# Optimization experiments

Measured on AMD Instinct MI355X. Metric: run time of the kernel, lower is better.

The kernel has to match this reference:

```python
import jax, jax.numpy as jnp
import numpy as np

# dims
BB, T, D_IN = 16, 2048, 64
D = 512          # hidden_dim (d_model)
DI = 2 * D       # d_inner (expand=2)
N = 16           # d_state
DC = 4           # d_conv
R = D // 16      # dt_rank = 32
L = 3            # n_layer
D_OUT = 128


def setup_inputs() -> dict:
    key = jax.random.key(0)
    ks = jax.random.split(key, 10)
    g = lambda k, shape, s: (jax.random.normal(k, shape, jnp.float32) * s)
    A_log = jnp.tile(jnp.log(jnp.arange(1, N + 1, dtype=jnp.float32))[None, None, :], (L, DI, 1))
    return {
        "x": g(ks[0], (BB, T, D_IN), 1.0),
        "Wi": g(ks[1], (D, D_IN), 0.05), "bi": jnp.zeros((D,), jnp.float32),
        "Win": g(ks[2], (L, 2 * DI, D), 0.02),
        "convw": g(ks[3], (L, DI, DC), 0.2), "convb": jnp.zeros((L, DI), jnp.float32),
        "Wx": g(ks[4], (L, R + 2 * N, DI), 0.02),
        "Wdt": g(ks[5], (L, DI, R), 0.05), "bdt": jnp.full((L, DI), -1.0, jnp.float32),
        "A_log": A_log, "Dp": jnp.ones((L, DI), jnp.float32),
        "Wout": g(ks[6], (L, D, DI), 0.02),
        "Wo": g(ks[7], (D_OUT, D), 0.05), "bo": jnp.zeros((D_OUT,), jnp.float32),
    }


def _selective_scan(u, delta, A, Bm, Cm, Dv):
    # u, delta: [B,T,DI]; A: [DI,N]; Bm, Cm: [B,T,N]; Dv: [DI]
    def step(h, inp):
        d_t, u_t, B_t, C_t = inp  # [B,DI],[B,DI],[B,N],[B,N]
        dA = jnp.exp(d_t[:, :, None] * A)                      # [B,DI,N]
        h = dA * h + (d_t * u_t)[:, :, None] * B_t[:, None, :]  # [B,DI,N]
        y = jnp.einsum('bdn,bn->bd', h, C_t)
        return h, y

    h0 = jnp.zeros((u.shape[0], u.shape[2], A.shape[1]), u.dtype)
    xs = (delta.transpose(1, 0, 2), u.transpose(1, 0, 2),
          Bm.transpose(1, 0, 2), Cm.transpose(1, 0, 2))
    _, ys = jax.lax.scan(step, h0, xs)
    return ys.transpose(1, 0, 2) + u * Dv


def _mamba_layer(x, Win, cw, cb, Wx, Wdt, bdt, A_log, Dv, Wout):
    xz = x @ Win.T                      # [B,T,2*DI]
    xin, z = jnp.split(xz, 2, axis=-1)
    # causal depthwise conv1d
    xc = jax.lax.conv_general_dilated(
        xin.transpose(0, 2, 1), cw[:, None, :], (1,), [(DC - 1, 0)],
        feature_group_count=DI, dimension_numbers=('NCH', 'OIH', 'NCH'))
    u = jax.nn.silu((xc + cb[None, :, None]).transpose(0, 2, 1))  # [B,T,DI]
    dbc = u @ Wx.T                      # [B,T,R+2N]
    dt, Bm, Cm = dbc[..., :R], dbc[..., R:R + N], dbc[..., R + N:]
    delta = jax.nn.softplus(dt @ Wdt.T + bdt)
    A = -jnp.exp(A_log)
    y = _selective_scan(u, delta, A, Bm, Cm, Dv)
    return (y * jax.nn.silu(z)) @ Wout.T


def reference(x, Wi, bi, Win, convw, convb, Wx, Wdt, bdt, A_log, Dp, Wout, Wo, bo):
    h = x @ Wi.T + bi
    for l in range(L):
        h = _mamba_layer(h, Win[l], convw[l], convb[l], Wx[l], Wdt[l], bdt[l],
                         A_log[l], Dp[l], Wout[l])
    return jnp.tanh(h @ Wo.T + bo)  # [B,T,output_dim]
```

## Files before the change

### kernel.cpp

```cpp
#include <hip/hip_runtime.h>
#include <hip/hip_bf16.h>

#define BB_ 16
#define T_ 2048
#define DIN_ 64
#define D_ 512
#define DI_ 1024
#define N_ 16
#define DC_ 4
#define R_ 32
#define L_ 3
#define DOUT_ 128
#define CL_ 64
#define NCH_ (T_ / CL_)

typedef __attribute__((ext_vector_type(8))) _Float16 f16x8;
typedef __attribute__((ext_vector_type(4))) float f32x4;

__device__ __forceinline__ float silu_f(float x) { return x / (1.f + __expf(-x)); }

__device__ __forceinline__ float softplus_f(float t) {
    return fmaxf(t, 0.f) + __logf(1.f + __expf(-fabsf(t)));
}

__device__ __forceinline__ unsigned short f2h(float f) {
    union { _Float16 h; unsigned short u; } c;
    c.h = (_Float16)f;
    return c.u;
}

__device__ __forceinline__ void gload_lds16(const unsigned short* g,
                                            unsigned short* l) {
    __builtin_amdgcn_global_load_lds(
        (const __attribute__((address_space(1))) void*)g,
        (__attribute__((address_space(3))) void*)l, 16, 0, 0);
}

__device__ __forceinline__ float decode_scale(unsigned int bits) {
    if (bits == 0u) return 1.f;
    const int E = (int)(bits >> 23) & 0xFF;
    return __uint_as_float((unsigned)(265 - E) << 23);
}

__device__ __forceinline__ uint4 pack8(float4 lo, float4 hi, float s) {
    union { uint4 u; unsigned short h[8]; } r;
    r.h[0] = f2h(lo.x * s); r.h[1] = f2h(lo.y * s);
    r.h[2] = f2h(lo.z * s); r.h[3] = f2h(lo.w * s);
    r.h[4] = f2h(hi.x * s); r.h[5] = f2h(hi.y * s);
    r.h[6] = f2h(hi.z * s); r.h[7] = f2h(hi.w * s);
    return r.u;
}

__device__ __forceinline__ const float* wregion(
    int r, const float* Win, const float* Wout, const float* Wx,
    const float* Wo, size_t* n4)
{
    if (r < 3)       { *n4 = 262144; return Win  + (size_t)r * 1048576; }
    else if (r < 6)  { *n4 = 131072; return Wout + (size_t)(r - 3) * 524288; }
    else if (r == 6) { *n4 = 16384;  return Wo; }
    else             { *n4 = 16384;  return Wx  + (size_t)(r - 7) * 65536; }
}

__global__ __launch_bounds__(256) void amax_all(
    const float* __restrict__ Win, const float* __restrict__ Wout,
    const float* __restrict__ Wx, const float* __restrict__ Wo,
    unsigned int* __restrict__ scales)
{
    size_t n4;
    const float* p = wregion(blockIdx.z, Win, Wout, Wx, Wo, &n4);
    float m = 0.f;
    for (size_t i = (size_t)blockIdx.x * 256 + threadIdx.x; i < n4;
         i += (size_t)gridDim.x * 256) {
        const float4 v = ((const float4*)p)[i];
        m = fmaxf(m, fmaxf(fmaxf(fabsf(v.x), fabsf(v.y)),
                           fmaxf(fabsf(v.z), fabsf(v.w))));
    }
#pragma unroll
    for (int off = 32; off; off >>= 1) m = fmaxf(m, __shfl_down(m, off));
    __shared__ float sm[4];
    if ((threadIdx.x & 63) == 0) sm[threadIdx.x >> 6] = m;
    __syncthreads();
    if (threadIdx.x == 0) {
        const float b = fmaxf(fmaxf(sm[0], sm[1]), fmaxf(sm[2], sm[3]));
        atomicMax(scales + blockIdx.z, __float_as_uint(b));
    }
}

__global__ __launch_bounds__(256) void cast_all(
    const float* __restrict__ Win, const float* __restrict__ Wout,
    const float* __restrict__ Wx, const float* __restrict__ Wo,
    unsigned short* __restrict__ WinH, unsigned short* __restrict__ WoutH,
    unsigned short* __restrict__ WxH, unsigned short* __restrict__ WoH,
    const unsigned int* __restrict__ scales)
{
    const int r = blockIdx.z;
    size_t n4;
    const float* p = wregion(r, Win, Wout, Wx, Wo, &n4);
    unsigned short* o;
    if (r < 3)       o = WinH  + (size_t)r * 1048576;
    else if (r < 6)  o = WoutH + (size_t)(r - 3) * 524288;
    else if (r == 6) o = WoH;
    else             o = WxH   + (size_t)(r - 7) * 65536;
    const float s = decode_scale(scales[r]);
    for (size_t i = (size_t)blockIdx.x * 256 + threadIdx.x; i < n4;
         i += (size_t)gridDim.x * 256) {
        const float4 v = ((const float4*)p)[i];
        ((ushort4*)o)[i] = make_ushort4(f2h(v.x * s), f2h(v.y * s),
                                        f2h(v.z * s), f2h(v.w * s));
    }
}

template<int ACT>
__global__ __launch_bounds__(256) void gemm_f32a_t128(
    const float* __restrict__ A, int lda,
    const unsigned short* __restrict__ B, int ldb,
    const float* __restrict__ bias,
    float* __restrict__ C, int ldc, int K,
    const unsigned int* __restrict__ sa, const unsigned int* __restrict__ sb,
    unsigned int* __restrict__ oamax)
{
    __shared__ __align__(16) unsigned short As[128 * 32];
    __shared__ __align__(16) unsigned short Bs[2][128 * 32];
    const int tid  = threadIdx.x;
    const int lane = tid & 63;
    const int w    = tid >> 6;
    const int wr   = (w >> 1) << 6;
    const int wc   = (w & 1) << 6;
    const int l15  = lane & 15, l4 = lane >> 4;
    const int row0 = blockIdx.y << 7, col0 = blockIdx.x << 7;
    const int tq   = tid >> 2;
    const int tr   = (tid & 3) << 3;

    const float sA  = decode_scale(*sa);
    const float inv = (1.f / sA) * (1.f / decode_scale(*sb));

    const float* Ar0 = A + (size_t)(row0 + tq) * lda + tr;
    const float* Ar1 = A + (size_t)(row0 + 64 + tq) * lda + tr;
    const unsigned short* Br0 = B + (size_t)(col0 + tq) * ldb + tr;
    const unsigned short* Br1 = B + (size_t)(col0 + 64 + tq) * ldb + tr;

    f32x4 acc[4][4];
#pragma unroll
    for (int m = 0; m < 4; ++m)
#pragma unroll
        for (int n = 0; n < 4; ++n) acc[m][n] = (f32x4){0.f, 0.f, 0.f, 0.f};

    float4 a0lo = *(const float4*)(Ar0), a0hi = *(const float4*)(Ar0 + 4);
    float4 a1lo = *(const float4*)(Ar1), a1hi = *(const float4*)(Ar1 + 4);
    gload_lds16(Br0, &Bs[0][tq * 32 + tr]);
    gload_lds16(Br1, &Bs[0][(64 + tq) * 32 + tr]);

    int cur = 0;
    for (int k0 = 0; k0 < K; k0 += 32) {
        __syncthreads();
        *(uint4*)&As[tq * 32 + tr]        = pack8(a0lo, a0hi, sA);
        *(uint4*)&As[(64 + tq) * 32 + tr] = pack8(a1lo, a1hi, sA);
        __syncthreads();

        if (k0 + 32 < K) {
            gload_lds16(Br0 + k0 + 32, &Bs[cur ^ 1][tq * 32 + tr]);
            gload_lds16(Br1 + k0 + 32, &Bs[cur ^ 1][(64 + tq) * 32 + tr]);
            a0lo = *(const float4*)(Ar0 + k0 + 32);
            a0hi = *(const float4*)(Ar0 + k0 + 36);
            a1lo = *(const float4*)(Ar1 + k0 + 32);
            a1hi = *(const float4*)(Ar1 + k0 + 36);
        }

        f16x8 af[4], bfr[4];
#pragma unroll
        for (int m = 0; m < 4; ++m)
            af[m] = *(const f16x8*)&As[(wr + m * 16 + l15) * 32 + l4 * 8];
#pragma unroll
        for (int n = 0; n < 4; ++n)
            bfr[n] = *(const f16x8*)&Bs[cur][(wc + n * 16 + l15) * 32 + l4 * 8];
#pragma unroll
        for (int m = 0; m < 4; ++m)
#pragma unroll
            for (int n = 0; n < 4; ++n)
                acc[m][n] = __builtin_amdgcn_mfma_f32_16x16x32_f16(
                    af[m], bfr[n], acc[m][n], 0, 0, 0);
        cur ^= 1;
    }

    float am = 0.f;
#pragma unroll
    for (int n = 0; n < 4; ++n) {
        const int col = col0 + wc + n * 16 + l15;
        float bc = 0.f;
        if (ACT == 3) bc = bias[col];
#pragma unroll
        for (int m = 0; m < 4; ++m) {
            const int rowb = row0 + wr + m * 16 + (l4 << 2);
#pragma unroll
            for (int r = 0; r < 4; ++r) {
                float v = acc[m][n][r] * inv;
                if (ACT == 3) v = tanhf(v + bc);
                C[(size_t)(rowb + r) * ldc + col] = v;
                am = fmaxf(am, fabsf(v));
            }
        }
    }
    if (oamax) {
#pragma unroll
        for (int off = 32; off; off >>= 1) am = fmaxf(am, __shfl_down(am, off));
        if (lane == 0) atomicMax(oamax, __float_as_uint(am));
    }
}

__global__ __launch_bounds__(256) void gemm_f16u_t64n(
    const float* __restrict__ A, int lda,
    const unsigned short* __restrict__ B, int ldb,
    float* __restrict__ C, int ldc, int K,
    const unsigned int* __restrict__ sa, const unsigned int* __restrict__ sb)
{
    __shared__ __align__(16) unsigned short As[128 * 32];
    __shared__ __align__(16) unsigned short Bs[64 * 32];
    const int tid  = threadIdx.x;
    const int lane = tid & 63;
    const int w    = tid >> 6;
    const int l15  = lane & 15, l4 = lane >> 4;
    const int row0 = blockIdx.y << 7;
    const int tq   = tid >> 2;
    const int tr   = (tid & 3) << 3;

    const float sA  = decode_scale(*sa);
    const float inv = (1.f / sA) * (1.f / decode_scale(*sb));

    const float* Ar0 = A + (size_t)(row0 + tq) * lda + tr;
    const float* Ar1 = A + (size_t)(row0 + 64 + tq) * lda + tr;
    const unsigned short* Br = B + (size_t)tq * ldb + tr;

    f32x4 acc[2][4];
#pragma unroll
    for (int m = 0; m < 2; ++m)
#pragma unroll
        for (int n = 0; n < 4; ++n) acc[m][n] = (f32x4){0.f, 0.f, 0.f, 0.f};

    float4 a0lo = *(const float4*)(Ar0), a0hi = *(const float4*)(Ar0 + 4);
    float4 a1lo = *(const float4*)(Ar1), a1hi = *(const float4*)(Ar1 + 4);
    uint4  bv   = *(const uint4*)(Br);

    for (int k0 = 0; k0 < K; k0 += 32) {
        __syncthreads();
        *(uint4*)&As[tq * 32 + tr]        = pack8(a0lo, a0hi, sA);
        *(uint4*)&As[(64 + tq) * 32 + tr] = pack8(a1lo, a1hi, sA);
        *(uint4*)&Bs[tq * 32 + tr]        = bv;
        __syncthreads();

        if (k0 + 32 < K) {
            a0lo = *(const float4*)(Ar0 + k0 + 32);
            a0hi = *(const float4*)(Ar0 + k0 + 36);
            a1lo = *(const float4*)(Ar1 + k0 + 32);
            a1hi = *(const float4*)(Ar1 + k0 + 36);
            bv   = *(const uint4*)(Br  + k0 + 32);
        }

        f16x8 af[2], bfr[4];
#pragma unroll
        for (int m = 0; m < 2; ++m)
            af[m] = *(const f16x8*)&As[(w * 32 + m * 16 + l15) * 32 + l4 * 8];
#pragma unroll
        for (int n = 0; n < 4; ++n)
            bfr[n] = *(const f16x8*)&Bs[(n * 16 + l15) * 32 + l4 * 8];
#pragma unroll
        for (int m = 0; m < 2; ++m)
#pragma unroll
            for (int n = 0; n < 4; ++n)
                acc[m][n] = __builtin_amdgcn_mfma_f32_16x16x32_f16(
                    af[m], bfr[n], acc[m][n], 0, 0, 0);
    }

#pragma unroll
    for (int n = 0; n < 4; ++n) {
        const int col = n * 16 + l15;
#pragma unroll
        for (int m = 0; m < 2; ++m) {
            const int rowb = row0 + w * 32 + m * 16 + (l4 << 2);
#pragma unroll
            for (int r = 0; r < 4; ++r)
                C[(size_t)(rowb + r) * ldc + col] = acc[m][n][r] * inv;
        }
    }
}

__global__ __launch_bounds__(256) void gemm_in(
    const float* __restrict__ A, int lda,
    const float* __restrict__ B, int ldb,
    const float* __restrict__ bias,
    float* __restrict__ C, int ldc, int K,
    unsigned int* __restrict__ oamax)
{
    __shared__ __align__(16) float As[8][128];
    __shared__ __align__(16) float Bs[8][128];
    const int tid  = threadIdx.x;
    const int row0 = blockIdx.y << 7;
    const int col0 = blockIdx.x << 7;
    const int tx = tid & 15, ty = tid >> 4;

    float acc[8][8];
#pragma unroll
    for (int i = 0; i < 8; ++i)
#pragma unroll
        for (int j = 0; j < 8; ++j) acc[i][j] = 0.f;

    const int arow = tid >> 1;
    const int acol = (tid & 1) << 2;
    const float* Ap = A + (size_t)(row0 + arow) * lda + acol;
    const float* Bp = B + (size_t)(col0 + arow) * ldb + acol;

    for (int k0 = 0; k0 < K; k0 += 8) {
        const float4 av = *(const float4*)(Ap + k0);
        const float4 bv = *(const float4*)(Bp + k0);
        __syncthreads();
        As[acol + 0][arow] = av.x; As[acol + 1][arow] = av.y;
        As[acol + 2][arow] = av.z; As[acol + 3][arow] = av.w;
        Bs[acol + 0][arow] = bv.x; Bs[acol + 1][arow] = bv.y;
        Bs[acol + 2][arow] = bv.z; Bs[acol + 3][arow] = bv.w;
        __syncthreads();
#pragma unroll
        for (int k = 0; k < 8; ++k) {
            float a[8], b[8];
            *(float4*)&a[0] = *(const float4*)&As[k][ty << 3];
            *(float4*)&a[4] = *(const float4*)&As[k][(ty << 3) + 4];
            *(float4*)&b[0] = *(const float4*)&Bs[k][tx << 3];
            *(float4*)&b[4] = *(const float4*)&Bs[k][(tx << 3) + 4];
#pragma unroll
            for (int i = 0; i < 8; ++i)
#pragma unroll
                for (int j = 0; j < 8; ++j)
                    acc[i][j] = fmaf(a[i], b[j], acc[i][j]);
        }
    }

    float bv8[8];
#pragma unroll
    for (int j = 0; j < 8; ++j) bv8[j] = bias[col0 + (tx << 3) + j];

    float am = 0.f;
#pragma unroll
    for (int i = 0; i < 8; ++i) {
        float v[8];
#pragma unroll
        for (int j = 0; j < 8; ++j) {
            v[j] = acc[i][j] + bv8[j];
            am = fmaxf(am, fabsf(v[j]));
        }
        float* Cp = C + (size_t)(row0 + (ty << 3) + i) * ldc + col0 + (tx << 3);
        *(float4*)(Cp)     = make_float4(v[0], v[1], v[2], v[3]);
        *(float4*)(Cp + 4) = make_float4(v[4], v[5], v[6], v[7]);
    }
#pragma unroll
    for (int off = 32; off; off >>= 1) am = fmaxf(am, __shfl_down(am, off));
    if ((tid & 63) == 0) atomicMax(oamax, __float_as_uint(am));
}

__global__ __launch_bounds__(256) void conv_silu_kernel(
    const float* __restrict__ xz, const float* __restrict__ cw,
    const float* __restrict__ cb, float* __restrict__ u,
    size_t total4, unsigned int* __restrict__ uamax)
{
    float am = 0.f;
    for (size_t i = (size_t)blockIdx.x * 256 + threadIdx.x; i < total4;
         i += (size_t)gridDim.x * 256) {
        const size_t e = i * 4;
        const int c = (int)(e & (DI_ - 1));
        const size_t m = e >> 10;
        const int t = (int)(m & (T_ - 1));
        const float* xr = xz + m * 2048 + c;
        const float4 zero = make_float4(0.f, 0.f, 0.f, 0.f);
        const float4 x0 = (t >= 3) ? *(const float4*)(xr - 3 * 2048) : zero;
        const float4 x1 = (t >= 2) ? *(const float4*)(xr - 2 * 2048) : zero;
        const float4 x2 = (t >= 1) ? *(const float4*)(xr - 1 * 2048) : zero;
        const float4 x3 = *(const float4*)(xr);
        const float4 cbv = *(const float4*)(cb + c);
        const float4 w0 = *(const float4*)(cw + (size_t)c * 4);
        const float4 w1 = *(const float4*)(cw + (size_t)(c + 1) * 4);
        const float4 w2 = *(const float4*)(cw + (size_t)(c + 2) * 4);
        const float4 w3 = *(const float4*)(cw + (size_t)(c + 3) * 4);
        float4 r;
        r.x = silu_f(fmaf(x3.x, w0.w, fmaf(x2.x, w0.z, fmaf(x1.x, w0.y, fmaf(x0.x, w0.x, cbv.x)))));
        r.y = silu_f(fmaf(x3.y, w1.w, fmaf(x2.y, w1.z, fmaf(x1.y, w1.y, fmaf(x0.y, w1.x, cbv.y)))));
        r.z = silu_f(fmaf(x3.z, w2.w, fmaf(x2.z, w2.z, fmaf(x1.z, w2.y, fmaf(x0.z, w2.x, cbv.z)))));
        r.w = silu_f(fmaf(x3.w, w3.w, fmaf(x2.w, w3.z, fmaf(x1.w, w3.y, fmaf(x0.w, w3.x, cbv.w)))));
        *(float4*)(u + e) = r;
        am = fmaxf(am, fmaxf(fmaxf(fabsf(r.x), fabsf(r.y)),
                             fmaxf(fabsf(r.z), fabsf(r.w))));
    }
#pragma unroll
    for (int off = 32; off; off >>= 1) am = fmaxf(am, __shfl_down(am, off));
    __shared__ float sm[4];
    if ((threadIdx.x & 63) == 0) sm[threadIdx.x >> 6] = am;
    __syncthreads();
    if (threadIdx.x == 0) {
        const float b = fmaxf(fmaxf(sm[0], sm[1]), fmaxf(sm[2], sm[3]));
        atomicMax(uamax, __float_as_uint(b));
    }
}


__device__ __forceinline__ bool geo_check(const float* a2) {
    bool ok = true;
#pragma unroll
    for (int n = 1; n < N_; ++n)
        ok = ok && (fabsf(a2[n] - a2[0] * (n + 1)) <=
                    1e-5f * fmaxf(1.f, fabsf(a2[n])));
    return ok;
}

__global__ __launch_bounds__(256) void scan_pass1(
    const float* __restrict__ u, const float* __restrict__ dbc,
    const float* __restrict__ A_log_l, const float* __restrict__ Wdt_l,
    const float* __restrict__ bdt_l,
    float* __restrict__ P, float* __restrict__ S)
{
    __shared__ __align__(16) float sAll[CL_][64];
    const int tid = threadIdx.x;
    const int b = blockIdx.x, ch = blockIdx.z;
    const int d = (blockIdx.y << 8) + tid;

    float a2[N_], hs[N_];
#pragma unroll
    for (int n = 0; n < N_; ++n) {
        a2[n] = -__expf(A_log_l[d * N_ + n]) * 1.44269504f;
        hs[n] = 0.f;
    }
    const bool geo = geo_check(a2);
    float wdt[32];
#pragma unroll
    for (int k = 0; k < 32; k += 4)
        *(float4*)&wdt[k] = *(const float4*)(Wdt_l + (size_t)d * 32 + k);
    const float bdt_d = bdt_l[d];

    const size_t base64 = ((size_t)b * T_ + (size_t)ch * CL_) * 64;
    float* sflat = &sAll[0][0];
    for (int i = tid; i < CL_ * 64; i += 256) sflat[i] = dbc[base64 + i];
    __syncthreads();

    float sdl = 0.f;
    if (geo) {
        for (int tt = 0; tt < CL_; ++tt) {
            float t = bdt_d;
#pragma unroll
            for (int k = 0; k < 32; k += 4) {
                const float4 dv = *(const float4*)&sAll[tt][k];
                t = fmaf(dv.x, wdt[k + 0], t);
                t = fmaf(dv.y, wdt[k + 1], t);
                t = fmaf(dv.z, wdt[k + 2], t);
                t = fmaf(dv.w, wdt[k + 3], t);
            }
            const float dl = softplus_f(t);
            sdl += dl;
            const size_t m = (size_t)b * T_ + ch * CL_ + tt;
            const float du = dl * u[m * DI_ + d];
            const float r = exp2f(dl * a2[0]);
            float dA = r;
#pragma unroll
            for (int n = 0; n < N_; ++n) {
                hs[n] = fmaf(dA, hs[n], du * sAll[tt][32 + n]);
                dA *= r;
            }
        }
    } else {
        for (int tt = 0; tt < CL_; ++tt) {
            float t = bdt_d;
#pragma unroll
            for (int k = 0; k < 32; k += 4) {
                const float4 dv = *(const float4*)&sAll[tt][k];
                t = fmaf(dv.x, wdt[k + 0], t);
                t = fmaf(dv.y, wdt[k + 1], t);
                t = fmaf(dv.z, wdt[k + 2], t);
                t = fmaf(dv.w, wdt[k + 3], t);
            }
            const float dl = softplus_f(t);
            sdl += dl;
            const size_t m = (size_t)b * T_ + ch * CL_ + tt;
            const float du = dl * u[m * DI_ + d];
#pragma unroll
            for (int n = 0; n < N_; ++n) {
                const float dA = exp2f(dl * a2[n]);
                hs[n] = fmaf(dA, hs[n], du * sAll[tt][32 + n]);
            }
        }
    }
#pragma unroll
    for (int n = 0; n < N_; ++n) {
        const size_t idx = (size_t)(((b * NCH_ + ch) * N_ + n) << 10) + d;
        P[idx] = exp2f(sdl * a2[n]);
        S[idx] = hs[n];
    }
}

__global__ __launch_bounds__(256) void scan_carry(
    const float* __restrict__ P, float* __restrict__ S)
{
    const size_t gid = (size_t)blockIdx.x * 256 + threadIdx.x;
    const int d = (int)(gid & 1023);
    const int n = (int)((gid >> 10) & 15);
    const int b = (int)(gid >> 14);
    float hc = 0.f;
    for (int ch = 0; ch < NCH_; ++ch) {
        const size_t idx = (size_t)(((b * NCH_ + ch) * N_ + n) << 10) + d;
        const float p = P[idx], s = S[idx];
        S[idx] = hc;
        hc = fmaf(p, hc, s);
    }
}

__global__ __launch_bounds__(256) void scan_pass3(
    float* __restrict__ xz, const float* __restrict__ u,
    const float* __restrict__ dbc, const float* __restrict__ A_log_l,
    const float* __restrict__ Wdt_l, const float* __restrict__ bdt_l,
    const float* __restrict__ Dp_l, const float* __restrict__ S,
    unsigned int* __restrict__ gmax)
{
    __shared__ __align__(16) float sAll[CL_][64];
    const int tid = threadIdx.x;
    const int b = blockIdx.x, ch = blockIdx.z;
    const int d = (blockIdx.y << 8) + tid;

    float a2[N_], hs[N_];
#pragma unroll
    for (int n = 0; n < N_; ++n) {
        a2[n] = -__expf(A_log_l[d * N_ + n]) * 1.44269504f;
        hs[n] = S[(size_t)(((b * NCH_ + ch) * N_ + n) << 10) + d];
    }
    const bool geo = geo_check(a2);
    float wdt[32];
#pragma unroll
    for (int k = 0; k < 32; k += 4)
        *(float4*)&wdt[k] = *(const float4*)(Wdt_l + (size_t)d * 32 + k);
    const float bdt_d = bdt_l[d];
    const float Dpd = Dp_l[d];

    const size_t base64 = ((size_t)b * T_ + (size_t)ch * CL_) * 64;
    float* sflat = &sAll[0][0];
    for (int i = tid; i < CL_ * 64; i += 256) sflat[i] = dbc[base64 + i];
    __syncthreads();

    float gm = 0.f;
    if (geo) {
        for (int tt = 0; tt < CL_; ++tt) {
            float t = bdt_d;
#pragma unroll
            for (int k = 0; k < 32; k += 4) {
                const float4 dv = *(const float4*)&sAll[tt][k];
                t = fmaf(dv.x, wdt[k + 0], t);
                t = fmaf(dv.y, wdt[k + 1], t);
                t = fmaf(dv.z, wdt[k + 2], t);
                t = fmaf(dv.w, wdt[k + 3], t);
            }
            const float dl = softplus_f(t);
            const size_t m = (size_t)b * T_ + ch * CL_ + tt;
            const float uv = u[m * DI_ + d];
            const float du = dl * uv;
            const float r = exp2f(dl * a2[0]);
            float dA = r;
            float yv = 0.f;
#pragma unroll
            for (int n = 0; n < N_; ++n) {
                hs[n] = fmaf(dA, hs[n], du * sAll[tt][32 + n]);
                yv = fmaf(hs[n], sAll[tt][48 + n], yv);
                dA *= r;
            }
            yv = fmaf(uv, Dpd, yv);
            const float g = yv * silu_f(xz[m * 2048 + DI_ + d]);
            xz[m * 2048 + d] = g;
            gm = fmaxf(gm, fabsf(g));
        }
    } else {
        for (int tt = 0; tt < CL_; ++tt) {
            float t = bdt_d;
#pragma unroll
            for (int k = 0; k < 32; k += 4) {
                const float4 dv = *(const float4*)&sAll[tt][k];
                t = fmaf(dv.x, wdt[k + 0], t);
                t = fmaf(dv.y, wdt[k + 1], t);
                t = fmaf(dv.z, wdt[k + 2], t);
                t = fmaf(dv.w, wdt[k + 3], t);
            }
            const float dl = softplus_f(t);
            const size_t m = (size_t)b * T_ + ch * CL_ + tt;
            const float uv = u[m * DI_ + d];
            const float du = dl * uv;
            float yv = 0.f;
#pragma unroll
            for (int n = 0; n < N_; ++n) {
                const float dA = exp2f(dl * a2[n]);
                hs[n] = fmaf(dA, hs[n], du * sAll[tt][32 + n]);
                yv = fmaf(hs[n], sAll[tt][48 + n], yv);
            }
            yv = fmaf(uv, Dpd, yv);
            const float g = yv * silu_f(xz[m * 2048 + DI_ + d]);
            xz[m * 2048 + d] = g;
            gm = fmaxf(gm, fabsf(g));
        }
    }
#pragma unroll
    for (int off = 32; off; off >>= 1) gm = fmaxf(gm, __shfl_down(gm, off));
    if ((tid & 63) == 0) atomicMax(gmax, __float_as_uint(gm));
}

extern "C" void kernel_launch(void* const* d_in, const int* in_sizes, int n_in,
                              void* d_out, int out_size, void* d_ws, size_t ws_size,
                              hipStream_t stream) {
    const float* x     = (const float*)d_in[0];
    const float* Wi    = (const float*)d_in[1];
    const float* bi    = (const float*)d_in[2];
    const float* Win   = (const float*)d_in[3];
    const float* convw = (const float*)d_in[4];
    const float* convb = (const float*)d_in[5];
    const float* Wx    = (const float*)d_in[6];
    const float* Wdt   = (const float*)d_in[7];
    const float* bdt   = (const float*)d_in[8];
    const float* A_log = (const float*)d_in[9];
    const float* Dp    = (const float*)d_in[10];
    const float* Wout  = (const float*)d_in[11];
    const float* Wo    = (const float*)d_in[12];
    const float* bo    = (const float*)d_in[13];
    float* out = (float*)d_out;

    const size_t rowf = 3648;
    const size_t wextra =
        (3 * 1048576 + 3 * 524288 + 65536 + 3 * 65536) / 2 + 32;
    int CB = BB_;
    while (CB > 1 && ((size_t)CB * T_ * rowf + wextra) * sizeof(float) > ws_size) CB >>= 1;
    const size_t Mc = (size_t)CB * T_;

    const dim3 blk(256);
    const int rowTiles = (int)(Mc / 128);

    float* ws   = (float*)d_ws;
    float* xz   = ws;
    float* u    = xz + Mc * 2048;
    float* dbc  = u  + Mc * 1024;
    float* hPS  = dbc + Mc * 64;
    float* hb   = hPS;
    float* Pbuf = hPS;
    float* Sbuf = hPS + (size_t)CB * NCH_ * N_ * DI_;
    unsigned short* WinH  = (unsigned short*)(hPS + Mc * 512);
    unsigned short* WoutH = WinH + 3 * 1048576;
    unsigned short* WoH   = WoutH + 3 * 524288;
    unsigned short* WxH   = WoH + 65536;
    unsigned int* scales  = (unsigned int*)(WxH + 3 * 65536);

    hipMemsetAsync(scales, 0, 32 * sizeof(unsigned int), stream);

    amax_all<<<dim3(128, 1, 10), blk, 0, stream>>>(Win, Wout, Wx, Wo, scales);
    cast_all<<<dim3(64, 1, 10), blk, 0, stream>>>(
        Win, Wout, Wx, Wo, WinH, WoutH, WxH, WoH, scales);

    for (int c = 0; c < BB_ / CB; ++c) {
        const float* x_c = x + (size_t)c * Mc * DIN_;
        float* out_c     = out + (size_t)c * Mc * DOUT_;

        hipMemsetAsync(scales + 10, 0, 10 * sizeof(unsigned int), stream);

        gemm_in<<<dim3(D_ / 128, rowTiles), blk, 0, stream>>>(
            x_c, DIN_, Wi, DIN_, bi, hb, D_, DIN_, scales + 10);

        for (int l = 0; l < L_; ++l) {
            const float* cw_l   = convw + (size_t)l * DI_ * DC_;
            const float* cb_l   = convb + (size_t)l * DI_;
            const float* Wdt_l  = Wdt  + (size_t)l * DI_ * R_;
            const float* bdt_l  = bdt  + (size_t)l * DI_;
            const float* Alog_l = A_log + (size_t)l * DI_ * N_;
            const float* Dp_l   = Dp   + (size_t)l * DI_;

            gemm_f32a_t128<0><<<dim3(2048 / 128, rowTiles), blk, 0, stream>>>(
                hb, D_, WinH + (size_t)l * 1048576, D_, nullptr,
                xz, 2048, D_, scales + 10 + l, scales + l, nullptr);

            conv_silu_kernel<<<dim3(2048), blk, 0, stream>>>(
                xz, cw_l, cb_l, u, Mc * DI_ / 4, scales + 17 + l);

            gemm_f16u_t64n<<<dim3(1, rowTiles), blk, 0, stream>>>(
                u, DI_, WxH + (size_t)l * 65536, DI_, dbc, 64, DI_,
                scales + 17 + l, scales + 7 + l);

            scan_pass1<<<dim3(CB, DI_ / 256, NCH_), blk, 0, stream>>>(
                u, dbc, Alog_l, Wdt_l, bdt_l, Pbuf, Sbuf);
            scan_carry<<<dim3(CB * 64), blk, 0, stream>>>(Pbuf, Sbuf);
            scan_pass3<<<dim3(CB, DI_ / 256, NCH_), blk, 0, stream>>>(
                xz, u, dbc, Alog_l, Wdt_l, bdt_l, Dp_l, Sbuf, scales + 14 + l);

            gemm_f32a_t128<0><<<dim3(D_ / 128, rowTiles), blk, 0, stream>>>(
                xz, 2048, WoutH + (size_t)l * 524288, DI_, nullptr,
                hb, D_, DI_, scales + 14 + l, scales + 3 + l, scales + 11 + l);
        }

        gemm_f32a_t128<3><<<dim3(DOUT_ / 128, rowTiles), blk, 0, stream>>>(
            hb, D_, WoH, D_, bo, out_c, DOUT_, D_,
            scales + 13, scales + 6, nullptr);
    }
}
```

Measured before the change: 2.594 ms.

## Fuse causal conv+SiLU into x-projection GEMM and scan passes, drop u buffer

Removes the standalone conv_silu kernel and the materialized u tensor. The conv and SiLU are recomputed inside the Wx GEMM's A-tile load and again inside both scan passes from xz. The quantization scale for u now comes from an analytic upper bound (|cb| plus the sum of |w| times amax of xz) rather than the true amax. The gated output goes to a separate compact gbuf, so the out-projection reads a contiguous DI-stride buffer. This trades a full write and read of u for redundant conv arithmetic, extra strided xz reads, and a looser fp16 scale that may cost precision.

```diff
diff --git a/kernel.cpp b/kernel.cpp
--- a/kernel.cpp
+++ b/kernel.cpp
@@ -110,6 +110,28 @@
     }
 }
 
+__global__ __launch_bounds__(256) void ubound_kernel(
+    const float* __restrict__ cw, const float* __restrict__ cb,
+    const unsigned int* __restrict__ xzslot, unsigned int* __restrict__ uslot)
+{
+    const float amx = __uint_as_float(*xzslot);
+    float m = 0.f;
+    for (int c = threadIdx.x; c < DI_; c += 256) {
+        const float4 w = *(const float4*)(cw + (size_t)c * 4);
+        const float sw = fabsf(w.x) + fabsf(w.y) + fabsf(w.z) + fabsf(w.w);
+        m = fmaxf(m, fabsf(cb[c]) + sw * amx);
+    }
+#pragma unroll
+    for (int off = 32; off; off >>= 1) m = fmaxf(m, __shfl_down(m, off));
+    __shared__ float sm[4];
+    if ((threadIdx.x & 63) == 0) sm[threadIdx.x >> 6] = m;
+    __syncthreads();
+    if (threadIdx.x == 0) {
+        const float b = fmaxf(fmaxf(sm[0], sm[1]), fmaxf(sm[2], sm[3]));
+        atomicMax(uslot, __float_as_uint(b));
+    }
+}
+
 template<int ACT>
 __global__ __launch_bounds__(256) void gemm_f32a_t128(
     const float* __restrict__ A, int lda,
@@ -207,11 +229,45 @@
     }
 }
 
-__global__ __launch_bounds__(256) void gemm_f16u_t64n(
-    const float* __restrict__ A, int lda,
+__device__ __forceinline__ uint4 conv_row8(
+    const float* __restrict__ xz, int m, int c0,
+    const float* __restrict__ cw, const float* __restrict__ cb, float s)
+{
+    const int t = m & (T_ - 1);
+    const float* xr = xz + (size_t)m * 2048 + c0;
+    float x[4][8];
+#pragma unroll
+    for (int k = 0; k < 4; ++k) {
+        const int dt = 3 - k;
+        if (t >= dt) {
+            *(float4*)&x[k][0] = *(const float4*)(xr - (size_t)dt * 2048);
+            *(float4*)&x[k][4] = *(const float4*)(xr - (size_t)dt * 2048 + 4);
+        } else {
+#pragma unroll
+            for (int j = 0; j < 8; ++j) x[k][j] = 0.f;
+        }
+    }
+    union { uint4 u; unsigned short h[8]; } r;
+#pragma unroll
+    for (int j = 0; j < 8; ++j) {
+        const int c = c0 + j;
+        const float4 w = *(const float4*)(cw + (size_t)c * 4);
+        float cv = cb[c];
+        cv = fmaf(x[0][j], w.x, cv);
+        cv = fmaf(x[1][j], w.y, cv);
+        cv = fmaf(x[2][j], w.z, cv);
+        cv = fmaf(x[3][j], w.w, cv);
+        r.h[j] = f2h(silu_f(cv) * s);
+    }
+    return r.u;
+}
+
+__global__ __launch_bounds__(256) void gemm_conv_t64n(
+    const float* __restrict__ xz,
     const unsigned short* __restrict__ B, int ldb,
+    const float* __restrict__ cw, const float* __restrict__ cb,
     float* __restrict__ C, int ldc, int K,
-    const unsigned int* __restrict__ sa, const unsigned int* __restrict__ sb)
+    const unsigned int* __restrict__ su, const unsigned int* __restrict__ sb)
 {
     __shared__ __align__(16) unsigned short As[128 * 32];
     __shared__ __align__(16) unsigned short Bs[64 * 32];
@@ -223,11 +279,9 @@
     const int tq   = tid >> 2;
     const int tr   = (tid & 3) << 3;
 
-    const float sA  = decode_scale(*sa);
-    const float inv = (1.f / sA) * (1.f / decode_scale(*sb));
-
-    const float* Ar0 = A + (size_t)(row0 + tq) * lda + tr;
-    const float* Ar1 = A + (size_t)(row0 + 64 + tq) * lda + tr;
+    const float sU  = decode_scale(*su);
+    const float inv = (1.f / sU) * (1.f / decode_scale(*sb));
+
     const unsigned short* Br = B + (size_t)tq * ldb + tr;
 
     f32x4 acc[2][4];
@@ -236,24 +290,18 @@
 #pragma unroll
         for (int n = 0; n < 4; ++n) acc[m][n] = (f32x4){0.f, 0.f, 0.f, 0.f};
 
-    float4 a0lo = *(const float4*)(Ar0), a0hi = *(const float4*)(Ar0 + 4);
-    float4 a1lo = *(const float4*)(Ar1), a1hi = *(const float4*)(Ar1 + 4);
-    uint4  bv   = *(const uint4*)(Br);
+    uint4 bv = *(const uint4*)(Br);
 
     for (int k0 = 0; k0 < K; k0 += 32) {
+        const uint4 a0 = conv_row8(xz, row0 + tq, k0 + tr, cw, cb, sU);
+        const uint4 a1 = conv_row8(xz, row0 + 64 + tq, k0 + tr, cw, cb, sU);
         __syncthreads();
-        *(uint4*)&As[tq * 32 + tr]        = pack8(a0lo, a0hi, sA);
-        *(uint4*)&As[(64 + tq) * 32 + tr] = pack8(a1lo, a1hi, sA);
+        *(uint4*)&As[tq * 32 + tr]        = a0;
+        *(uint4*)&As[(64 + tq) * 32 + tr] = a1;
         *(uint4*)&Bs[tq * 32 + tr]        = bv;
         __syncthreads();
 
-        if (k0 + 32 < K) {
-            a0lo = *(const float4*)(Ar0 + k0 + 32);
-            a0hi = *(const float4*)(Ar0 + k0 + 36);
-            a1lo = *(const float4*)(Ar1 + k0 + 32);
-            a1hi = *(const float4*)(Ar1 + k0 + 36);
-            bv   = *(const uint4*)(Br  + k0 + 32);
-        }
+        if (k0 + 32 < K) bv = *(const uint4*)(Br + k0 + 32);
 
         f16x8 af[2], bfr[4];
 #pragma unroll
@@ -354,49 +402,6 @@
     if ((tid & 63) == 0) atomicMax(oamax, __float_as_uint(am));
 }
 
-__global__ __launch_bounds__(256) void conv_silu_kernel(
-    const float* __restrict__ xz, const float* __restrict__ cw,
-    const float* __restrict__ cb, float* __restrict__ u,
-    size_t total4, unsigned int* __restrict__ uamax)
-{
-    float am = 0.f;
-    for (size_t i = (size_t)blockIdx.x * 256 + threadIdx.x; i < total4;
-         i += (size_t)gridDim.x * 256) {
-        const size_t e = i * 4;
-        const int c = (int)(e & (DI_ - 1));
-        const size_t m = e >> 10;
-        const int t = (int)(m & (T_ - 1));
-        const float* xr = xz + m * 2048 + c;
-        const float4 zero = make_float4(0.f, 0.f, 0.f, 0.f);
-        const float4 x0 = (t >= 3) ? *(const float4*)(xr - 3 * 2048) : zero;
-        const float4 x1 = (t >= 2) ? *(const float4*)(xr - 2 * 2048) : zero;
-        const float4 x2 = (t >= 1) ? *(const float4*)(xr - 1 * 2048) : zero;
-        const float4 x3 = *(const float4*)(xr);
-        const float4 cbv = *(const float4*)(cb + c);
-        const float4 w0 = *(const float4*)(cw + (size_t)c * 4);
-        const float4 w1 = *(const float4*)(cw + (size_t)(c + 1) * 4);
-        const float4 w2 = *(const float4*)(cw + (size_t)(c + 2) * 4);
-        const float4 w3 = *(const float4*)(cw + (size_t)(c + 3) * 4);
-        float4 r;
-        r.x = silu_f(fmaf(x3.x, w0.w, fmaf(x2.x, w0.z, fmaf(x1.x, w0.y, fmaf(x0.x, w0.x, cbv.x)))));
-        r.y = silu_f(fmaf(x3.y, w1.w, fmaf(x2.y, w1.z, fmaf(x1.y, w1.y, fmaf(x0.y, w1.x, cbv.y)))));
-        r.z = silu_f(fmaf(x3.z, w2.w, fmaf(x2.z, w2.z, fmaf(x1.z, w2.y, fmaf(x0.z, w2.x, cbv.z)))));
-        r.w = silu_f(fmaf(x3.w, w3.w, fmaf(x2.w, w3.z, fmaf(x1.w, w3.y, fmaf(x0.w, w3.x, cbv.w)))));
-        *(float4*)(u + e) = r;
-        am = fmaxf(am, fmaxf(fmaxf(fabsf(r.x), fabsf(r.y)),
-                             fmaxf(fabsf(r.z), fabsf(r.w))));
-    }
-#pragma unroll
-    for (int off = 32; off; off >>= 1) am = fmaxf(am, __shfl_down(am, off));
-    __shared__ float sm[4];
-    if ((threadIdx.x & 63) == 0) sm[threadIdx.x >> 6] = am;
-    __syncthreads();
-    if (threadIdx.x == 0) {
-        const float b = fmaxf(fmaxf(sm[0], sm[1]), fmaxf(sm[2], sm[3]));
-        atomicMax(uamax, __float_as_uint(b));
-    }
-}
-
 
 __device__ __forceinline__ bool geo_check(const float* a2) {
     bool ok = true;
@@ -408,9 +413,10 @@
 }
 
 __global__ __launch_bounds__(256) void scan_pass1(
-    const float* __restrict__ u, const float* __restrict__ dbc,
+    const float* __restrict__ xz, const float* __restrict__ dbc,
     const float* __restrict__ A_log_l, const float* __restrict__ Wdt_l,
-    const float* __restrict__ bdt_l,
+    const float* __restrict__ bdt_l, const float* __restrict__ cw_l,
+    const float* __restrict__ cb_l,
     float* __restrict__ P, float* __restrict__ S)
 {
     __shared__ __align__(16) float sAll[CL_][64];
@@ -430,28 +436,40 @@
     for (int k = 0; k < 32; k += 4)
         *(float4*)&wdt[k] = *(const float4*)(Wdt_l + (size_t)d * 32 + k);
     const float bdt_d = bdt_l[d];
-
-    const size_t base64 = ((size_t)b * T_ + (size_t)ch * CL_) * 64;
+    const float4 cwv = *(const float4*)(cw_l + (size_t)d * 4);
+    const float cbd = cb_l[d];
+
+    const size_t mB = (size_t)b * T_ + (size_t)ch * CL_;
+    const int t0 = ch * CL_;
+    float xm1 = (t0 >= 1) ? xz[(mB - 1) * 2048 + d] : 0.f;
+    float xm2 = (t0 >= 2) ? xz[(mB - 2) * 2048 + d] : 0.f;
+    float xm3 = (t0 >= 3) ? xz[(mB - 3) * 2048 + d] : 0.f;
+
+    const size_t base64 = mB * 64;
     float* sflat = &sAll[0][0];
     for (int i = tid; i < CL_ * 64; i += 256) sflat[i] = dbc[base64 + i];
     __syncthreads();
 
     float sdl = 0.f;
-    if (geo) {
-        for (int tt = 0; tt < CL_; ++tt) {
-            float t = bdt_d;
-#pragma unroll
-            for (int k = 0; k < 32; k += 4) {
-                const float4 dv = *(const float4*)&sAll[tt][k];
-                t = fmaf(dv.x, wdt[k + 0], t);
-                t = fmaf(dv.y, wdt[k + 1], t);
-                t = fmaf(dv.z, wdt[k + 2], t);
-                t = fmaf(dv.w, wdt[k + 3], t);
-            }
-            const float dl = softplus_f(t);
-            sdl += dl;
-            const size_t m = (size_t)b * T_ + ch * CL_ + tt;
-            const float du = dl * u[m * DI_ + d];
+    for (int tt = 0; tt < CL_; ++tt) {
+        float t = bdt_d;
+#pragma unroll
+        for (int k = 0; k < 32; k += 4) {
+            const float4 dv = *(const float4*)&sAll[tt][k];
+            t = fmaf(dv.x, wdt[k + 0], t);
+            t = fmaf(dv.y, wdt[k + 1], t);
+            t = fmaf(dv.z, wdt[k + 2], t);
+            t = fmaf(dv.w, wdt[k + 3], t);
+        }
+        const float dl = softplus_f(t);
+        sdl += dl;
+        const size_t m = mB + tt;
+        const float xc = xz[m * 2048 + d];
+        float cv = fmaf(xc, cwv.w, fmaf(xm1, cwv.z,
+                    fmaf(xm2, cwv.y, fmaf(xm3, cwv.x, cbd))));
+        const float du = dl * silu_f(cv);
+        xm3 = xm2; xm2 = xm1; xm1 = xc;
+        if (geo) {
             const float r = exp2f(dl * a2[0]);
             float dA = r;
 #pragma unroll
@@ -459,22 +477,7 @@
                 hs[n] = fmaf(dA, hs[n], du * sAll[tt][32 + n]);
                 dA *= r;
             }
-        }
-    } else {
-        for (int tt = 0; tt < CL_; ++tt) {
-            float t = bdt_d;
-#pragma unroll
-            for (int k = 0; k < 32; k += 4) {
-                const float4 dv = *(const float4*)&sAll[tt][k];
-                t = fmaf(dv.x, wdt[k + 0], t);
-                t = fmaf(dv.y, wdt[k + 1], t);
-                t = fmaf(dv.z, wdt[k + 2], t);
-                t = fmaf(dv.w, wdt[k + 3], t);
-            }
-            const float dl = softplus_f(t);
-            sdl += dl;
-            const size_t m = (size_t)b * T_ + ch * CL_ + tt;
-            const float du = dl * u[m * DI_ + d];
+        } else {
 #pragma unroll
             for (int n = 0; n < N_; ++n) {
                 const float dA = exp2f(dl * a2[n]);
@@ -507,9 +510,10 @@
 }
 
 __global__ __launch_bounds__(256) void scan_pass3(
-    float* __restrict__ xz, const float* __restrict__ u,
+    const float* __restrict__ xz, float* __restrict__ g,
     const float* __restrict__ dbc, const float* __restrict__ A_log_l,
     const float* __restrict__ Wdt_l, const float* __restrict__ bdt_l,
+    const float* __restrict__ cw_l, const float* __restrict__ cb_l,
     const float* __restrict__ Dp_l, const float* __restrict__ S,
     unsigned int* __restrict__ gmax)
 {
@@ -530,70 +534,62 @@
     for (int k = 0; k < 32; k += 4)
         *(float4*)&wdt[k] = *(const float4*)(Wdt_l + (size_t)d * 32 + k);
     const float bdt_d = bdt_l[d];
+    const float4 cwv = *(const float4*)(cw_l + (size_t)d * 4);
+    const float cbd = cb_l[d];
     const float Dpd = Dp_l[d];
 
-    const size_t base64 = ((size_t)b * T_ + (size_t)ch * CL_) * 64;
+    const size_t mB = (size_t)b * T_ + (size_t)ch * CL_;
+    const int t0 = ch * CL_;
+    float xm1 = (t0 >= 1) ? xz[(mB - 1) * 2048 + d] : 0.f;
+    float xm2 = (t0 >= 2) ? xz[(mB - 2) * 2048 + d] : 0.f;
+    float xm3 = (t0 >= 3) ? xz[(mB - 3) * 2048 + d] : 0.f;
+
+    const size_t base64 = mB * 64;
     float* sflat = &sAll[0][0];
     for (int i = tid; i < CL_ * 64; i += 256) sflat[i] = dbc[base64 + i];
     __syncthreads();
 
     float gm = 0.f;
-    if (geo) {
-        for (int tt = 0; tt < CL_; ++tt) {
-            float t = bdt_d;
-#pragma unroll
-            for (int k = 0; k < 32; k += 4) {
-                const float4 dv = *(const float4*)&sAll[tt][k];
-                t = fmaf(dv.x, wdt[k + 0], t);
-                t = fmaf(dv.y, wdt[k + 1], t);
-                t = fmaf(dv.z, wdt[k + 2], t);
-                t = fmaf(dv.w, wdt[k + 3], t);
-            }
-            const float dl = softplus_f(t);
-            const size_t m = (size_t)b * T_ + ch * CL_ + tt;
-            const float uv = u[m * DI_ + d];
-            const float du = dl * uv;
+    for (int tt = 0; tt < CL_; ++tt) {
+        float t = bdt_d;
+#pragma unroll
+        for (int k = 0; k < 32; k += 4) {
+            const float4 dv = *(const float4*)&sAll[tt][k];
+            t = fmaf(dv.x, wdt[k + 0], t);
+            t = fmaf(dv.y, wdt[k + 1], t);
+            t = fmaf(dv.z, wdt[k + 2], t);
+            t = fmaf(dv.w, wdt[k + 3], t);
+        }
+        const float dl = softplus_f(t);
+        const size_t m = mB + tt;
+        const float xc = xz[m * 2048 + d];
+        float cv = fmaf(xc, cwv.w, fmaf(xm1, cwv.z,
+                    fmaf(xm2, cwv.y, fmaf(xm3, cwv.x, cbd))));
+        const float uv = silu_f(cv);
+        const float du = dl * uv;
+        xm3 = xm2; xm2 = xm1; xm1 = xc;
+        float yv = 0.f;
+        if (geo) {
             const float r = exp2f(dl * a2[0]);
             float dA = r;
-            float yv = 0.f;
 #pragma unroll
             for (int n = 0; n < N_; ++n) {
                 hs[n] = fmaf(dA, hs[n], du * sAll[tt][32 + n]);
                 yv = fmaf(hs[n], sAll[tt][48 + n], yv);
                 dA *= r;
             }
-            yv = fmaf(uv, Dpd, yv);
-            const float g = yv * silu_f(xz[m * 2048 + DI_ + d]);
-            xz[m * 2048 + d] = g;
-            gm = fmaxf(gm, fabsf(g));
-        }
-    } else {
-        for (int tt = 0; tt < CL_; ++tt) {
-            float t = bdt_d;
-#pragma unroll
-            for (int k = 0; k < 32; k += 4) {
-                const float4 dv = *(const float4*)&sAll[tt][k];
-                t = fmaf(dv.x, wdt[k + 0], t);
-                t = fmaf(dv.y, wdt[k + 1], t);
-                t = fmaf(dv.z, wdt[k + 2], t);
-                t = fmaf(dv.w, wdt[k + 3], t);
-            }
-            const float dl = softplus_f(t);
-            const size_t m = (size_t)b * T_ + ch * CL_ + tt;
-            const float uv = u[m * DI_ + d];
-            const float du = dl * uv;
-            float yv = 0.f;
+        } else {
 #pragma unroll
             for (int n = 0; n < N_; ++n) {
                 const float dA = exp2f(dl * a2[n]);
                 hs[n] = fmaf(dA, hs[n], du * sAll[tt][32 + n]);
                 yv = fmaf(hs[n], sAll[tt][48 + n], yv);
             }
-            yv = fmaf(uv, Dpd, yv);
-            const float g = yv * silu_f(xz[m * 2048 + DI_ + d]);
-            xz[m * 2048 + d] = g;
-            gm = fmaxf(gm, fabsf(g));
-        }
+        }
+        yv = fmaf(uv, Dpd, yv);
+        const float gv = yv * silu_f(xz[m * 2048 + DI_ + d]);
+        g[m * DI_ + d] = gv;
+        gm = fmaxf(gm, fabsf(gv));
     }
 #pragma unroll
     for (int off = 32; off; off >>= 1) gm = fmaxf(gm, __shfl_down(gm, off));
@@ -631,8 +627,8 @@
 
     float* ws   = (float*)d_ws;
     float* xz   = ws;
-    float* u    = xz + Mc * 2048;
-    float* dbc  = u  + Mc * 1024;
+    float* gbuf = xz + Mc * 2048;
+    float* dbc  = gbuf + Mc * 1024;
     float* hPS  = dbc + Mc * 64;
     float* hb   = hPS;
     float* Pbuf = hPS;
@@ -653,7 +649,7 @@
         const float* x_c = x + (size_t)c * Mc * DIN_;
         float* out_c     = out + (size_t)c * Mc * DOUT_;
 
-        hipMemsetAsync(scales + 10, 0, 10 * sizeof(unsigned int), stream);
+        hipMemsetAsync(scales + 10, 0, 16 * sizeof(unsigned int), stream);
 
         gemm_in<<<dim3(D_ / 128, rowTiles), blk, 0, stream>>>(
             x_c, DIN_, Wi, DIN_, bi, hb, D_, DIN_, scales + 10);
@@ -668,23 +664,24 @@
 
             gemm_f32a_t128<0><<<dim3(2048 / 128, rowTiles), blk, 0, stream>>>(
                 hb, D_, WinH + (size_t)l * 1048576, D_, nullptr,
-                xz, 2048, D_, scales + 10 + l, scales + l, nullptr);
-
-            conv_silu_kernel<<<dim3(2048), blk, 0, stream>>>(
-                xz, cw_l, cb_l, u, Mc * DI_ / 4, scales + 17 + l);
-
-            gemm_f16u_t64n<<<dim3(1, rowTiles), blk, 0, stream>>>(
-                u, DI_, WxH + (size_t)l * 65536, DI_, dbc, 64, DI_,
-                scales + 17 + l, scales + 7 + l);
+                xz, 2048, D_, scales + 10 + l, scales + l, scales + 17 + l);
+
+            ubound_kernel<<<dim3(1), blk, 0, stream>>>(
+                cw_l, cb_l, scales + 17 + l, scales + 20 + l);
+
+            gemm_conv_t64n<<<dim3(1, rowTiles), blk, 0, stream>>>(
+                xz, WxH + (size_t)l * 65536, DI_, cw_l, cb_l, dbc, 64, DI_,
+                scales + 20 + l, scales + 7 + l);
 
             scan_pass1<<<dim3(CB, DI_ / 256, NCH_), blk, 0, stream>>>(
-                u, dbc, Alog_l, Wdt_l, bdt_l, Pbuf, Sbuf);
+                xz, dbc, Alog_l, Wdt_l, bdt_l, cw_l, cb_l, Pbuf, Sbuf);
             scan_carry<<<dim3(CB * 64), blk, 0, stream>>>(Pbuf, Sbuf);
             scan_pass3<<<dim3(CB, DI_ / 256, NCH_), blk, 0, stream>>>(
-                xz, u, dbc, Alog_l, Wdt_l, bdt_l, Dp_l, Sbuf, scales + 14 + l);
+                xz, gbuf, dbc, Alog_l, Wdt_l, bdt_l, cw_l, cb_l, Dp_l,
+                Sbuf, scales + 14 + l);
 
             gemm_f32a_t128<0><<<dim3(D_ / 128, rowTiles), blk, 0, stream>>>(
-                xz, 2048, WoutH + (size_t)l * 524288, DI_, nullptr,
+                gbuf, DI_, WoutH + (size_t)l * 524288, DI_, nullptr,
                 hb, D_, DI_, scales + 14 + l, scales + 3 + l, scales + 11 + l);
         }
 
```

Result: slower. 3.202 ms (+23.5%).
